# Optimization experiments

Hardware: AMD Instinct MI355X
Metric: run time of the kernel (lower is better)

The kernel has to match this reference:

```python
import jax, jax.numpy as jnp
import numpy as np

NUM_GROUPS = 32
EPS = 1e-6


def group_norm(x, gamma, beta):
    # x: (B, C, H, W), 32 groups, eps=1e-6, affine
    B, C, H, W = x.shape
    xg = x.reshape(B, NUM_GROUPS, C // NUM_GROUPS, H, W)
    mean = xg.mean(axis=(2, 3, 4), keepdims=True)
    var = xg.var(axis=(2, 3, 4), keepdims=True)
    xn = ((xg - mean) * jax.lax.rsqrt(var + EPS)).reshape(B, C, H, W)
    return xn * gamma[None, :, None, None] + beta[None, :, None, None]


def conv1x1(x, w, b):
    # 1x1 conv == channel matmul. x: (B,C,H,W), w: (O,C), b: (O,)
    return jnp.einsum('bchw,oc->bohw', x, w) + b[None, :, None, None]


def setup_inputs() -> dict:
    key = jax.random.key(0)
    B, C, H, W = 16, 512, 32, 32
    ks = jax.random.split(key, 12)
    s = 1.0 / np.sqrt(C)
    return {
        'x': jax.random.normal(ks[0], (B, C, H, W), dtype=jnp.float32),
        'gn_gamma': jnp.ones((C,), dtype=jnp.float32),
        'gn_beta': jnp.zeros((C,), dtype=jnp.float32),
        'wq': jax.random.normal(ks[1], (C, C), dtype=jnp.float32) * s,
        'bq': jnp.zeros((C,), dtype=jnp.float32),
        'wk': jax.random.normal(ks[2], (C, C), dtype=jnp.float32) * s,
        'bk': jnp.zeros((C,), dtype=jnp.float32),
        'wv': jax.random.normal(ks[3], (C, C), dtype=jnp.float32) * s,
        'bv': jnp.zeros((C,), dtype=jnp.float32),
        'wp': jax.random.normal(ks[4], (C, C), dtype=jnp.float32) * s,
        'bp': jnp.zeros((C,), dtype=jnp.float32),
    }


def reference(x, gn_gamma, gn_beta, wq, bq, wk, bk, wv, bv, wp, bp):
    B, C, H, W = x.shape
    residual = x
    xn = group_norm(x, gn_gamma, gn_beta)
    q = conv1x1(xn, wq, bq).reshape(B, C, H * W)  # (B, C, HW)
    k = conv1x1(xn, wk, bk).reshape(B, C, H * W)
    v = conv1x1(xn, wv, bv).reshape(B, C, H * W)
    scale = C ** (-0.5)
    # energy[b,i,j] = q_i . k_j
    energy = jnp.einsum('bci,bcj->bij', q, k) * scale
    attn = jax.nn.softmax(energy, axis=-1)
    # out[b,c,i] = sum_j attn[b,i,j] * v[b,c,j]
    out = jnp.einsum('bij,bcj->bci', attn, v).reshape(B, C, H, W)
    out = conv1x1(out, wp, bp)
    return out + residual
```

## Files before the change

kernel.cpp:

```cpp
#include <hip/hip_runtime.h>
#include <hip/hip_bf16.h>

using bf16 = __hip_bfloat16;

typedef __attribute__((ext_vector_type(8))) __bf16 bf16x8;
typedef __attribute__((ext_vector_type(4))) float floatx4;

#define EPS 1e-6f

#define RAW_BARRIER()  asm volatile("s_barrier" ::: "memory")
#define WAIT_VM16()    asm volatile("s_waitcnt vmcnt(16)" ::: "memory")
#define WAIT_VM8()     asm volatile("s_waitcnt vmcnt(8)" ::: "memory")
#define WAIT_VM4()     asm volatile("s_waitcnt vmcnt(4)" ::: "memory")
#define WAIT_VM0()     asm volatile("s_waitcnt vmcnt(0)" ::: "memory")
#define SCHED_FENCE()  __builtin_amdgcn_sched_barrier(0)
#define PRIO1()        __builtin_amdgcn_s_setprio(1)
#define PRIO0()        __builtin_amdgcn_s_setprio(0)

__device__ __forceinline__ void load_lds16(const void* g, void* l) {
    __builtin_amdgcn_global_load_lds(
        (const __attribute__((address_space(1))) void*)g,
        (__attribute__((address_space(3))) void*)l, 16, 0, 0);
}

__device__ __forceinline__ void storeOut(float* p, float v) { *p = v; }
__device__ __forceinline__ void storeOut(bf16* p, float v) { *p = __float2bfloat16(v); }

#define MFMA16(a, b, c) __builtin_amdgcn_mfma_f32_16x16x32_bf16(a, b, c, 0, 0, 0)

template <int BIAS_MODE, int RESID_EN, int QKV, typename OutT>
__global__ __launch_bounds__(256, 2) void gemm2b(
    const bf16* __restrict__ A, long long aStride, int lda,
    const bf16* __restrict__ B, long long bStride, int ldb,
    OutT* __restrict__ D, long long dStride, int ldd,
    bf16* __restrict__ vout, long long vStride,
    const float* __restrict__ bias,
    const float* __restrict__ resid, long long rStride, int ldr,
    int K, int tpb, int gx)
{
    constexpr int HB = 8192;
    extern __shared__ char smem[];

    const unsigned chunk = gridDim.x >> 3;
    const unsigned glob  = (blockIdx.x & 7) * chunk + (blockIdx.x >> 3);
    const unsigned z  = glob / (unsigned)tpb;
    const unsigned t  = glob % (unsigned)tpb;
    const int m0 = (int)(t / (unsigned)gx) << 7;
    const int n0 = (int)(t % (unsigned)gx) << 7;

    const int tid  = threadIdx.x;
    const int lane = tid & 63;
    const int wave = tid >> 6;
    const int wm   = wave >> 1;
    const int wn   = wave & 1;

    const bf16* Ab = A + (size_t)z * aStride + (size_t)m0 * lda;
    const bf16* Bb = B + (size_t)z * bStride + (size_t)n0 * ldb;

    floatx4 acc[4][4];
#pragma unroll
    for (int i = 0; i < 4; ++i)
#pragma unroll
        for (int j = 0; j < 4; ++j) acc[i][j] = (floatx4){0.f, 0.f, 0.f, 0.f};

    const int laneRow = lane & 15;
    const int laneKq  = lane >> 4;
    const int kqs16   = (laneKq ^ ((laneRow >> 1) & 3)) << 4;
    const int arow0   = wm * 64 + laneRow;
    const int brow0   = wn * 64 + laneRow;

    auto stage = [&](int kt, int h) {
        char* Adst = smem + ((kt & 1) * 2 + h) * HB;
        char* Bdst = smem + 4 * HB + ((kt & 1) * 2 + h) * HB;
        const int kb = (kt << 6) + (h << 5);
#pragma unroll
        for (int u = 0; u < 2; ++u) {
            const int idx = tid + u * 256;
            const int r  = idx >> 2;
            const int qs = (idx & 3) ^ ((idx >> 3) & 3);
            load_lds16(Ab + (size_t)r * lda + kb + qs * 8, Adst + idx * 16);
        }
#pragma unroll
        for (int u = 0; u < 2; ++u) {
            const int idx = tid + u * 256;
            const int r  = idx >> 2;
            const int qs = (idx & 3) ^ ((idx >> 3) & 3);
            load_lds16(Bb + (size_t)r * ldb + kb + qs * 8, Bdst + idx * 16);
        }
    };

    const int nt = K >> 6;
    stage(0, 0); stage(0, 1); stage(1, 0);

    for (int kt = 0; kt < nt; ++kt) {
        const char* Ablk = smem + (kt & 1) * 2 * HB;
        const char* Bblk = smem + 4 * HB + (kt & 1) * 2 * HB;
        const bool lastT = (kt == nt - 1);

        if (lastT) WAIT_VM4(); else WAIT_VM8();
        RAW_BARRIER();
        bf16x8 af[4], bfr[4];
#pragma unroll
        for (int im = 0; im < 4; ++im)
            af[im] = *(const bf16x8*)(Ablk + (arow0 + im * 16) * 64 + kqs16);
#pragma unroll
        for (int in = 0; in < 4; ++in)
            bfr[in] = *(const bf16x8*)(Bblk + (brow0 + in * 16) * 64 + kqs16);
        if (kt + 1 < nt) stage(kt + 1, 1);
        RAW_BARRIER();
        PRIO1();
#pragma unroll
        for (int im = 0; im < 4; ++im)
#pragma unroll
            for (int in = 0; in < 4; ++in)
                acc[im][in] = MFMA16(af[im], bfr[in], acc[im][in]);
        PRIO0();

        if (lastT) WAIT_VM0(); else WAIT_VM8();
        RAW_BARRIER();
#pragma unroll
        for (int im = 0; im < 4; ++im)
            af[im] = *(const bf16x8*)(Ablk + HB + (arow0 + im * 16) * 64 + kqs16);
#pragma unroll
        for (int in = 0; in < 4; ++in)
            bfr[in] = *(const bf16x8*)(Bblk + HB + (brow0 + in * 16) * 64 + kqs16);
        if (kt + 2 < nt) stage(kt + 2, 0);
        RAW_BARRIER();
        PRIO1();
#pragma unroll
        for (int im = 0; im < 4; ++im)
#pragma unroll
            for (int in = 0; in < 4; ++in)
                acc[im][in] = MFMA16(af[im], bfr[in], acc[im][in]);
        PRIO0();
    }

    const size_t dbase = (size_t)z * dStride;
#pragma unroll
    for (int im = 0; im < 4; ++im) {
        const int gmb = m0 + wm * 64 + im * 16 + (laneKq << 2);
#pragma unroll
        for (int in = 0; in < 4; ++in) {
            const int gn = n0 + wn * 64 + in * 16 + laneRow;
            float bn = 0.f;
            if (BIAS_MODE == 2) bn = bias[gn];
            if (QKV && n0 >= 1024) {
                union { bf16 h[4]; ushort4 u; } pk;
#pragma unroll
                for (int r = 0; r < 4; ++r)
                    pk.h[r] = __float2bfloat16(acc[im][in][r] + bn);
                *(ushort4*)(vout + (size_t)z * vStride +
                            (size_t)(gn - 1024) * 1024 + gmb) = pk.u;
            } else {
#pragma unroll
                for (int r = 0; r < 4; ++r) {
                    const int gm = gmb + r;
                    float v = acc[im][in][r];
                    if (BIAS_MODE == 1) v += bias[gm];
                    if (BIAS_MODE == 2) v += bn;
                    if (RESID_EN)
                        v += resid[(size_t)z * rStride + (size_t)gm * ldr + gn];
                    storeOut(D + dbase + (size_t)gm * ldd + gn, v);
                }
            }
        }
    }
}

__global__ __launch_bounds__(256, 1) void fattn(
    const bf16* __restrict__ qkT,
    const bf16* __restrict__ vv,
    bf16* __restrict__ O2,
    float scale)
{
    constexpr int KT = 32768;
    extern __shared__ char smem[];
    __shared__ __align__(16) char plds[4 * 1024];
    __shared__ float rsLDS[64];

    const int bid  = blockIdx.x;
    const int glob = (bid & 7) * 32 + (bid >> 3);
    const int b    = glob >> 4;
    const int i0   = (glob & 15) << 6;

    const int tid     = threadIdx.x;
    const int lane    = tid & 63;
    const int wave    = tid >> 6;
    const int laneRow = lane & 15;
    const int laneKq  = lane >> 4;
    const int kqs16   = (laneKq ^ ((laneRow >> 1) & 3)) << 4;

    const bf16* Qb = qkT + (size_t)b * 1048576 + (size_t)(i0 + wave * 16) * 1024;
    const bf16* Kb = qkT + (size_t)b * 1048576 + 512;
    const bf16* Vb = vv + (size_t)b * 524288;

    bf16x8 qf[16];
#pragma unroll
    for (int ks = 0; ks < 16; ++ks)
        qf[ks] = *(const bf16x8*)(Qb + (size_t)laneRow * 1024 + ks * 32 + laneKq * 8);

    floatx4 acc[8][4];
#pragma unroll
    for (int mf = 0; mf < 8; ++mf)
#pragma unroll
        for (int ni = 0; ni < 4; ++ni) acc[mf][ni] = (floatx4){0.f, 0.f, 0.f, 0.f};
    float rs = 0.f;

    auto stageK = [&](int jt) {
        char* dst = smem + (jt & 1) * KT;
        const bf16* src = Kb + ((size_t)jt << 5) * 1024;
#pragma unroll
        for (int u = 0; u < 8; ++u) {
            const int idx = tid + u * 256;
            const int kk = idx >> 7;
            const int j  = (idx >> 2) & 31;
            const int p  = idx & 3;
            load_lds16(src + (size_t)j * 1024 + kk * 32 + 8 * (p ^ ((j >> 1) & 3)),
                       dst + idx * 16);
        }
    };
    auto stageV = [&](int jt) {
        char* dst = smem + 2 * KT + (jt & 1) * KT;
        const bf16* src = Vb + (jt << 5);
#pragma unroll
        for (int u = 0; u < 8; ++u) {
            const int idx = tid + u * 256;
            const int c = idx >> 2;
            const int p = idx & 3;
            load_lds16(src + (size_t)c * 1024 + 8 * (p ^ ((c >> 1) & 3)),
                       dst + idx * 16);
        }
    };

    stageK(0); stageV(0); stageK(1); stageV(1);

    char* plw = plds + wave * 1024 + laneRow * 64;
    const int sw2 = ((laneRow >> 1) & 3) << 1;

    for (int jt = 0; jt < 32; ++jt) {
        if (jt == 31) WAIT_VM0(); else WAIT_VM16();
        RAW_BARRIER();
        const char* Kt = smem + (jt & 1) * KT;
        const char* Vt = smem + 2 * KT + (jt & 1) * KT;

        floatx4 s0 = (floatx4){0.f, 0.f, 0.f, 0.f};
        floatx4 s1 = (floatx4){0.f, 0.f, 0.f, 0.f};
#pragma unroll
        for (int ks = 0; ks < 16; ++ks) {
            bf16x8 kf0 = *(const bf16x8*)(Kt + ks * 2048 + laneRow * 64 + kqs16);
            bf16x8 kf1 = *(const bf16x8*)(Kt + ks * 2048 + (laneRow + 16) * 64 + kqs16);
            s0 = MFMA16(kf0, qf[ks], s0);
            s1 = MFMA16(kf1, qf[ks], s1);
        }

        union { bf16 h[4]; unsigned long long u; } w0, w1;
#pragma unroll
        for (int r = 0; r < 4; ++r) {
            float v0 = __expf(s0[r] * scale);
            float v1 = __expf(s1[r] * scale);
            rs += v0 + v1;
            w0.h[r] = __float2bfloat16(v0);
            w1.h[r] = __float2bfloat16(v1);
        }
        *(unsigned long long*)(plw + ((laneKq)     ^ sw2) * 8) = w0.u;
        *(unsigned long long*)(plw + ((laneKq + 4) ^ sw2) * 8) = w1.u;
        asm volatile("s_waitcnt lgkmcnt(0)" ::: "memory");
        RAW_BARRIER();
        SCHED_FENCE();
        bf16x8 pf[4];
#pragma unroll
        for (int ni = 0; ni < 4; ++ni)
            pf[ni] = *(const bf16x8*)(plds + ni * 1024 + laneRow * 64 + kqs16);

        PRIO1();
#pragma unroll
        for (int mf = 0; mf < 8; ++mf) {
            bf16x8 vf = *(const bf16x8*)(Vt +
                (wave * 128 + mf * 16 + laneRow) * 64 + kqs16);
#pragma unroll
            for (int ni = 0; ni < 4; ++ni)
                acc[mf][ni] = MFMA16(vf, pf[ni], acc[mf][ni]);
        }
        PRIO0();

        RAW_BARRIER();
        if (jt + 2 < 32) { stageK(jt + 2); stageV(jt + 2); }
    }

    rs += __shfl_xor(rs, 16);
    rs += __shfl_xor(rs, 32);
    if (lane < 16) rsLDS[wave * 16 + lane] = rs;
    __syncthreads();

#pragma unroll
    for (int ni = 0; ni < 4; ++ni) {
        const float ri = 1.f / rsLDS[ni * 16 + laneRow];
        bf16* Ob = O2 + (size_t)b * 524288 +
                   (size_t)(i0 + ni * 16 + laneRow) * 512 +
                   wave * 128 + (laneKq << 2);
#pragma unroll
        for (int mf = 0; mf < 8; ++mf) {
            union { bf16 h[4]; ushort4 u; } pk;
#pragma unroll
            for (int r = 0; r < 4; ++r)
                pk.h[r] = __float2bfloat16(acc[mf][ni][r] * ri);
            *(ushort4*)(Ob + mf * 16) = pk.u;
        }
    }
}

__global__ __launch_bounds__(256) void gn_stats(const float* __restrict__ x,
                                                float* __restrict__ stats)
{
    const int bg = blockIdx.x;
    const float4* p = (const float4*)(x + (size_t)bg * 16384);
    float s = 0.f, ss = 0.f;
    for (int i = threadIdx.x; i < 4096; i += 256) {
        float4 v = p[i];
        s  += v.x + v.y + v.z + v.w;
        ss += v.x * v.x + v.y * v.y + v.z * v.z + v.w * v.w;
    }
#pragma unroll
    for (int off = 32; off; off >>= 1) {
        s  += __shfl_down(s, off);
        ss += __shfl_down(ss, off);
    }
    __shared__ float rsm[4], rss[4];
    const int wv = threadIdx.x >> 6;
    if ((threadIdx.x & 63) == 0) { rsm[wv] = s; rss[wv] = ss; }
    __syncthreads();
    if (threadIdx.x == 0) {
        float S  = rsm[0] + rsm[1] + rsm[2] + rsm[3];
        float SS = rss[0] + rss[1] + rss[2] + rss[3];
        float mean = S * (1.f / 16384.f);
        float var  = SS * (1.f / 16384.f) - mean * mean;
        stats[2 * bg]     = mean;
        stats[2 * bg + 1] = rsqrtf(var + EPS);
    }
}

__global__ __launch_bounds__(256) void gn_apply_t(const float* __restrict__ x,
                                                  const float* __restrict__ stats,
                                                  const float* __restrict__ gamma,
                                                  const float* __restrict__ beta,
                                                  bf16* __restrict__ xnT)
{
    __shared__ bf16 tile[32][36];
    const int b = blockIdx.z, c0 = blockIdx.y * 32, i0 = blockIdx.x * 32;
    {
        const int cc = threadIdx.x >> 3;
        const int i4 = (threadIdx.x & 7) << 2;
        const int c  = c0 + cc;
        const float mean = stats[2 * ((b << 5) + (c >> 4))];
        const float rstd = stats[2 * ((b << 5) + (c >> 4)) + 1];
        const float a  = gamma[c] * rstd;
        const float bb = beta[c] - mean * a;
        float4 v = *(const float4*)(x + (((size_t)(b * 512 + c)) << 10) + i0 + i4);
        tile[cc][i4 + 0] = __float2bfloat16(v.x * a + bb);
        tile[cc][i4 + 1] = __float2bfloat16(v.y * a + bb);
        tile[cc][i4 + 2] = __float2bfloat16(v.z * a + bb);
        tile[cc][i4 + 3] = __float2bfloat16(v.w * a + bb);
    }
    __syncthreads();
    {
        const int ii = threadIdx.x >> 3;
        const int c4 = (threadIdx.x & 7) << 2;
        union { bf16 h[4]; uint2 u; } pk;
        pk.h[0] = tile[c4 + 0][ii];
        pk.h[1] = tile[c4 + 1][ii];
        pk.h[2] = tile[c4 + 2][ii];
        pk.h[3] = tile[c4 + 3][ii];
        *((uint2*)(xnT + (((size_t)(b * 1024 + i0 + ii)) << 9) + c0 + c4)) = pk.u;
    }
}

__global__ __launch_bounds__(256) void prep(
    const float* __restrict__ wq, const float* __restrict__ wk,
    const float* __restrict__ wv, const float* __restrict__ wp,
    bf16* __restrict__ wqkvb, bf16* __restrict__ wpb,
    const float* __restrict__ bq, const float* __restrict__ bk,
    const float* __restrict__ bv, float* __restrict__ bqkv)
{
    const int id = blockIdx.x;
    if (id < 1024) {
        const int w = id >> 8;
        const float* src = (w == 0) ? wq : (w == 1) ? wk : (w == 2) ? wv : wp;
        bf16* dst = (w < 3) ? (wqkvb + (size_t)w * 262144) : wpb;
        const int g = (id & 255) * 256 + threadIdx.x;
        float4 v = ((const float4*)src)[g];
        union { bf16 h[4]; uint2 u; } pk;
        pk.h[0] = __float2bfloat16(v.x);
        pk.h[1] = __float2bfloat16(v.y);
        pk.h[2] = __float2bfloat16(v.z);
        pk.h[3] = __float2bfloat16(v.w);
        ((uint2*)dst)[g] = pk.u;
    } else {
        for (int t = threadIdx.x; t < 1536; t += 256)
            bqkv[t] = (t < 512) ? bq[t] : (t < 1024) ? bk[t - 512] : bv[t - 1024];
    }
}

extern "C" void kernel_launch(void* const* d_in, const int* in_sizes, int n_in,
                              void* d_out, int out_size, void* d_ws, size_t ws_size,
                              hipStream_t stream)
{
    const float* x     = (const float*)d_in[0];
    const float* gamma = (const float*)d_in[1];
    const float* beta  = (const float*)d_in[2];
    const float* wq    = (const float*)d_in[3];
    const float* bq    = (const float*)d_in[4];
    const float* wk    = (const float*)d_in[5];
    const float* bk    = (const float*)d_in[6];
    const float* wv    = (const float*)d_in[7];
    const float* bv    = (const float*)d_in[8];
    const float* wp    = (const float*)d_in[9];
    const float* bp    = (const float*)d_in[10];
    float* out = (float*)d_out;

    char* ws = (char*)d_ws;
    size_t off = 0;
    auto alloc = [&](size_t bytes) -> char* {
        char* p = ws + off;
        off += (bytes + 255) & ~(size_t)255;
        return p;
    };

    const long long S  = 1024, C = 512;
    const long long BS = S * C;
    const long long ES = S * S;

    float* stats  = (float*)alloc(512 * 2 * sizeof(float));
    float* bqkv   = (float*)alloc(1536 * sizeof(float));
    bf16* wqkvb = (bf16*)alloc((size_t)3 * C * C * 2);
    bf16* wpb   = (bf16*)alloc((size_t)C * C * 2);
    bf16* xnT   = (bf16*)alloc((size_t)16 * BS * 2);
    bf16* qkT   = (bf16*)alloc((size_t)16 * ES * 2);
    bf16* vv    = (bf16*)alloc((size_t)16 * BS * 2);
    bf16* O2    = (bf16*)alloc((size_t)16 * BS * 2);

    hipFuncSetAttribute((const void*)gemm2b<2, 0, 1, bf16>,
                        hipFuncAttributeMaxDynamicSharedMemorySize, 65536);
    hipFuncSetAttribute((const void*)gemm2b<1, 1, 0, float>,
                        hipFuncAttributeMaxDynamicSharedMemorySize, 65536);
    hipFuncSetAttribute((const void*)fattn,
                        hipFuncAttributeMaxDynamicSharedMemorySize, 131072);

    prep<<<1025, 256, 0, stream>>>(wq, wk, wv, wp, wqkvb, wpb, bq, bk, bv, bqkv);

    gn_stats<<<512, 256, 0, stream>>>(x, stats);
    gn_apply_t<<<dim3(32, 16, 16), 256, 0, stream>>>(x, stats, gamma, beta, xnT);

    gemm2b<2, 0, 1, bf16><<<1536, 256, 65536, stream>>>(
        xnT, BS, 512, wqkvb, 0, 512, qkT, ES, 1024, vv, BS,
        bqkv, nullptr, 0, 0, 512, 96, 12);

    const float scale = 0.044194173824159216f;
    fattn<<<256, 256, 131072, stream>>>(qkT, vv, O2, scale);

    gemm2b<1, 1, 0, float><<<512, 256, 65536, stream>>>(
        wpb, 0, 512, O2, BS, 512, out, BS, 1024, nullptr, 0,
        bp, x, BS, 1024, 512, 32, 8);
}
```

Before: 238.5 us.

## Halve attention query tile, load V directly to registers, double occupancy

The attention kernel now processes 32 query rows per block instead of 64 and launches 512 blocks. The four waves split into two query halves and two key halves, and the softmax row sums from the two key halves are added at the end. V fragments are loaded from global memory straight into registers rather than staged through LDS, which halves dynamic shared memory to 64 KB and allows two blocks per CU. The trade is that each K tile is reused over fewer queries and V reads from global are less coalesced, in exchange for more resident waves to hide latency.

```diff
diff --git a/kernel.cpp b/kernel.cpp
--- a/kernel.cpp
+++ b/kernel.cpp
@@ -167,7 +167,7 @@
     }
 }
 
-__global__ __launch_bounds__(256, 1) void fattn(
+__global__ __launch_bounds__(256, 2) void fattn(
     const bf16* __restrict__ qkT,
     const bf16* __restrict__ vv,
     bf16* __restrict__ O2,
@@ -175,35 +175,40 @@
 {
     constexpr int KT = 32768;
     extern __shared__ char smem[];
-    __shared__ __align__(16) char plds[4 * 1024];
-    __shared__ float rsLDS[64];
+    __shared__ __align__(16) char plds[2048];
+    __shared__ float rsLDS[2][32];
 
     const int bid  = blockIdx.x;
-    const int glob = (bid & 7) * 32 + (bid >> 3);
-    const int b    = glob >> 4;
-    const int i0   = (glob & 15) << 6;
+    const int glob = (bid & 7) * 64 + (bid >> 3);
+    const int b    = glob >> 5;
+    const int i0   = (glob & 31) << 5;
 
     const int tid     = threadIdx.x;
     const int lane    = tid & 63;
     const int wave    = tid >> 6;
+    const int jh      = wave >> 1;
+    const int ih      = wave & 1;
     const int laneRow = lane & 15;
     const int laneKq  = lane >> 4;
     const int kqs16   = (laneKq ^ ((laneRow >> 1) & 3)) << 4;
-
-    const bf16* Qb = qkT + (size_t)b * 1048576 + (size_t)(i0 + wave * 16) * 1024;
+    const int sw2     = ((laneRow >> 1) & 3) << 1;
+
+    const bf16* Qb = qkT + (size_t)b * 1048576 +
+                     (size_t)(i0 + ih * 16 + laneRow) * 1024;
     const bf16* Kb = qkT + (size_t)b * 1048576 + 512;
-    const bf16* Vb = vv + (size_t)b * 524288;
+    const bf16* Vb = vv + (size_t)b * 524288 +
+                     (size_t)(wave * 128 + laneRow) * 1024 + laneKq * 8;
 
     bf16x8 qf[16];
 #pragma unroll
     for (int ks = 0; ks < 16; ++ks)
-        qf[ks] = *(const bf16x8*)(Qb + (size_t)laneRow * 1024 + ks * 32 + laneKq * 8);
-
-    floatx4 acc[8][4];
+        qf[ks] = *(const bf16x8*)(Qb + ks * 32 + laneKq * 8);
+
+    floatx4 acc[8][2];
 #pragma unroll
     for (int mf = 0; mf < 8; ++mf)
 #pragma unroll
-        for (int ni = 0; ni < 4; ++ni) acc[mf][ni] = (floatx4){0.f, 0.f, 0.f, 0.f};
+        for (int ni = 0; ni < 2; ++ni) acc[mf][ni] = (floatx4){0.f, 0.f, 0.f, 0.f};
     float rs = 0.f;
 
     auto stageK = [&](int jt) {
@@ -219,85 +224,75 @@
                        dst + idx * 16);
         }
     };
-    auto stageV = [&](int jt) {
-        char* dst = smem + 2 * KT + (jt & 1) * KT;
-        const bf16* src = Vb + (jt << 5);
-#pragma unroll
-        for (int u = 0; u < 8; ++u) {
-            const int idx = tid + u * 256;
-            const int c = idx >> 2;
-            const int p = idx & 3;
-            load_lds16(src + (size_t)c * 1024 + 8 * (p ^ ((c >> 1) & 3)),
-                       dst + idx * 16);
-        }
+
+    bf16x8 vf[8];
+    auto loadV = [&](int jt) {
+        const bf16* vs = Vb + (jt << 5);
+#pragma unroll
+        for (int mf = 0; mf < 8; ++mf)
+            vf[mf] = *(const bf16x8*)(vs + (size_t)mf * 16384);
     };
 
-    stageK(0); stageV(0); stageK(1); stageV(1);
-
-    char* plw = plds + wave * 1024 + laneRow * 64;
-    const int sw2 = ((laneRow >> 1) & 3) << 1;
+    stageK(0);
+    loadV(0);
+    SCHED_FENCE();
+    stageK(1);
 
     for (int jt = 0; jt < 32; ++jt) {
-        if (jt == 31) WAIT_VM0(); else WAIT_VM16();
+        if (jt == 31) WAIT_VM8(); else WAIT_VM16();
         RAW_BARRIER();
         const char* Kt = smem + (jt & 1) * KT;
-        const char* Vt = smem + 2 * KT + (jt & 1) * KT;
-
-        floatx4 s0 = (floatx4){0.f, 0.f, 0.f, 0.f};
-        floatx4 s1 = (floatx4){0.f, 0.f, 0.f, 0.f};
+
+        floatx4 s = (floatx4){0.f, 0.f, 0.f, 0.f};
 #pragma unroll
         for (int ks = 0; ks < 16; ++ks) {
-            bf16x8 kf0 = *(const bf16x8*)(Kt + ks * 2048 + laneRow * 64 + kqs16);
-            bf16x8 kf1 = *(const bf16x8*)(Kt + ks * 2048 + (laneRow + 16) * 64 + kqs16);
-            s0 = MFMA16(kf0, qf[ks], s0);
-            s1 = MFMA16(kf1, qf[ks], s1);
-        }
-
-        union { bf16 h[4]; unsigned long long u; } w0, w1;
+            bf16x8 kf = *(const bf16x8*)(Kt + ks * 2048 +
+                                         (jh * 16 + laneRow) * 64 + kqs16);
+            s = MFMA16(kf, qf[ks], s);
+        }
+
+        union { bf16 h[4]; unsigned long long u; } w;
 #pragma unroll
         for (int r = 0; r < 4; ++r) {
-            float v0 = __expf(s0[r] * scale);
-            float v1 = __expf(s1[r] * scale);
-            rs += v0 + v1;
-            w0.h[r] = __float2bfloat16(v0);
-            w1.h[r] = __float2bfloat16(v1);
-        }
-        *(unsigned long long*)(plw + ((laneKq)     ^ sw2) * 8) = w0.u;
-        *(unsigned long long*)(plw + ((laneKq + 4) ^ sw2) * 8) = w1.u;
+            float v = __expf(s[r] * scale);
+            rs += v;
+            w.h[r] = __float2bfloat16(v);
+        }
+        *(unsigned long long*)(plds + ih * 1024 + laneRow * 64 +
+                               (((4 * jh + laneKq)) ^ sw2) * 8) = w.u;
         asm volatile("s_waitcnt lgkmcnt(0)" ::: "memory");
         RAW_BARRIER();
         SCHED_FENCE();
-        bf16x8 pf[4];
-#pragma unroll
-        for (int ni = 0; ni < 4; ++ni)
-            pf[ni] = *(const bf16x8*)(plds + ni * 1024 + laneRow * 64 + kqs16);
+        bf16x8 pf0 = *(const bf16x8*)(plds + laneRow * 64 + kqs16);
+        bf16x8 pf1 = *(const bf16x8*)(plds + 1024 + laneRow * 64 + kqs16);
+
+        if (jt == 31) WAIT_VM0(); else WAIT_VM8();
 
         PRIO1();
 #pragma unroll
         for (int mf = 0; mf < 8; ++mf) {
-            bf16x8 vf = *(const bf16x8*)(Vt +
-                (wave * 128 + mf * 16 + laneRow) * 64 + kqs16);
-#pragma unroll
-            for (int ni = 0; ni < 4; ++ni)
-                acc[mf][ni] = MFMA16(vf, pf[ni], acc[mf][ni]);
+            acc[mf][0] = MFMA16(vf[mf], pf0, acc[mf][0]);
+            acc[mf][1] = MFMA16(vf[mf], pf1, acc[mf][1]);
         }
         PRIO0();
 
         RAW_BARRIER();
-        if (jt + 2 < 32) { stageK(jt + 2); stageV(jt + 2); }
+        if (jt + 1 < 32) loadV(jt + 1);
+        SCHED_FENCE();
+        if (jt + 2 < 32) stageK(jt + 2);
     }
 
     rs += __shfl_xor(rs, 16);
     rs += __shfl_xor(rs, 32);
-    if (lane < 16) rsLDS[wave * 16 + lane] = rs;
+    if (lane < 16) rsLDS[jh][ih * 16 + lane] = rs;
     __syncthreads();
 
 #pragma unroll
-    for (int ni = 0; ni < 4; ++ni) {
-        const float ri = 1.f / rsLDS[ni * 16 + laneRow];
+    for (int ni = 0; ni < 2; ++ni) {
+        const int row = ni * 16 + laneRow;
+        const float ri = 1.f / (rsLDS[0][row] + rsLDS[1][row]);
         bf16* Ob = O2 + (size_t)b * 524288 +
-                   (size_t)(i0 + ni * 16 + laneRow) * 512 +
-                   wave * 128 + (laneKq << 2);
+                   (size_t)(i0 + row) * 512 + wave * 128 + (laneKq << 2);
 #pragma unroll
         for (int mf = 0; mf < 8; ++mf) {
             union { bf16 h[4]; ushort4 u; } pk;
@@ -443,7 +438,7 @@
     hipFuncSetAttribute((const void*)gemm2b<1, 1, 0, float>,
                         hipFuncAttributeMaxDynamicSharedMemorySize, 65536);
     hipFuncSetAttribute((const void*)fattn,
-                        hipFuncAttributeMaxDynamicSharedMemorySize, 131072);
+                        hipFuncAttributeMaxDynamicSharedMemorySize, 65536);
 
     prep<<<1025, 256, 0, stream>>>(wq, wk, wv, wp, wqkvb, wpb, bq, bk, bv, bqkv);
 
@@ -455,7 +450,7 @@
         bqkv, nullptr, 0, 0, 512, 96, 12);
 
     const float scale = 0.044194173824159216f;
-    fattn<<<256, 256, 131072, stream>>>(qkT, vv, O2, scale);
+    fattn<<<512, 256, 65536, stream>>>(qkT, vv, O2, scale);
 
     gemm2b<1, 1, 0, float><<<512, 256, 65536, stream>>>(
         wpb, 0, 512, O2, BS, 512, out, BS, 1024, nullptr, 0,
```

Result: slower. 272.3 us (+14.2%).

## Split attention work across 8 waves per block instead of 4

Applied to the files above, without the earlier changes.

The fused attention kernel now runs 512 threads (8 waves) per block. Each wave pair splits the 32-key tile's QK^T in half and the PV output channels are spread over 8 waves, so per-wave accumulators drop from 8x4 to 4x4 fragments. Staging loads per thread halve and the vmcnt wait is adjusted to match. Row sums are combined from two halves through LDS. The aim is more latency hiding and lower register pressure, at the cost of more waves contending at the per-tile barriers and duplicated Q fragment loads.

```diff
diff --git a/kernel.cpp b/kernel.cpp
--- a/kernel.cpp
+++ b/kernel.cpp
@@ -9,7 +9,6 @@
 #define EPS 1e-6f
 
 #define RAW_BARRIER()  asm volatile("s_barrier" ::: "memory")
-#define WAIT_VM16()    asm volatile("s_waitcnt vmcnt(16)" ::: "memory")
 #define WAIT_VM8()     asm volatile("s_waitcnt vmcnt(8)" ::: "memory")
 #define WAIT_VM4()     asm volatile("s_waitcnt vmcnt(4)" ::: "memory")
 #define WAIT_VM0()     asm volatile("s_waitcnt vmcnt(0)" ::: "memory")
@@ -167,7 +166,7 @@
     }
 }
 
-__global__ __launch_bounds__(256, 1) void fattn(
+__global__ __launch_bounds__(512, 2) void fattn(
     const bf16* __restrict__ qkT,
     const bf16* __restrict__ vv,
     bf16* __restrict__ O2,
@@ -176,7 +175,7 @@
     constexpr int KT = 32768;
     extern __shared__ char smem[];
     __shared__ __align__(16) char plds[4 * 1024];
-    __shared__ float rsLDS[64];
+    __shared__ float rsLDS[2][64];
 
     const int bid  = blockIdx.x;
     const int glob = (bid & 7) * 32 + (bid >> 3);
@@ -186,22 +185,26 @@
     const int tid     = threadIdx.x;
     const int lane    = tid & 63;
     const int wave    = tid >> 6;
+    const int jh      = wave & 1;
+    const int ih      = wave >> 1;
     const int laneRow = lane & 15;
     const int laneKq  = lane >> 4;
     const int kqs16   = (laneKq ^ ((laneRow >> 1) & 3)) << 4;
-
-    const bf16* Qb = qkT + (size_t)b * 1048576 + (size_t)(i0 + wave * 16) * 1024;
+    const int sw2     = ((laneRow >> 1) & 3) << 1;
+
+    const bf16* Qb = qkT + (size_t)b * 1048576 +
+                     (size_t)(i0 + ih * 16 + laneRow) * 1024;
     const bf16* Kb = qkT + (size_t)b * 1048576 + 512;
     const bf16* Vb = vv + (size_t)b * 524288;
 
     bf16x8 qf[16];
 #pragma unroll
     for (int ks = 0; ks < 16; ++ks)
-        qf[ks] = *(const bf16x8*)(Qb + (size_t)laneRow * 1024 + ks * 32 + laneKq * 8);
-
-    floatx4 acc[8][4];
-#pragma unroll
-    for (int mf = 0; mf < 8; ++mf)
+        qf[ks] = *(const bf16x8*)(Qb + ks * 32 + laneKq * 8);
+
+    floatx4 acc[4][4];
+#pragma unroll
+    for (int mf = 0; mf < 4; ++mf)
 #pragma unroll
         for (int ni = 0; ni < 4; ++ni) acc[mf][ni] = (floatx4){0.f, 0.f, 0.f, 0.f};
     float rs = 0.f;
@@ -210,8 +213,8 @@
         char* dst = smem + (jt & 1) * KT;
         const bf16* src = Kb + ((size_t)jt << 5) * 1024;
 #pragma unroll
-        for (int u = 0; u < 8; ++u) {
-            const int idx = tid + u * 256;
+        for (int u = 0; u < 4; ++u) {
+            const int idx = tid + u * 512;
             const int kk = idx >> 7;
             const int j  = (idx >> 2) & 31;
             const int p  = idx & 3;
@@ -223,8 +226,8 @@
         char* dst = smem + 2 * KT + (jt & 1) * KT;
         const bf16* src = Vb + (jt << 5);
 #pragma unroll
-        for (int u = 0; u < 8; ++u) {
-            const int idx = tid + u * 256;
+        for (int u = 0; u < 4; ++u) {
+            const int idx = tid + u * 512;
             const int c = idx >> 2;
             const int p = idx & 3;
             load_lds16(src + (size_t)c * 1024 + 8 * (p ^ ((c >> 1) & 3)),
@@ -234,36 +237,29 @@
 
     stageK(0); stageV(0); stageK(1); stageV(1);
 
-    char* plw = plds + wave * 1024 + laneRow * 64;
-    const int sw2 = ((laneRow >> 1) & 3) << 1;
-
     for (int jt = 0; jt < 32; ++jt) {
-        if (jt == 31) WAIT_VM0(); else WAIT_VM16();
+        if (jt == 31) WAIT_VM0(); else WAIT_VM8();
         RAW_BARRIER();
         const char* Kt = smem + (jt & 1) * KT;
         const char* Vt = smem + 2 * KT + (jt & 1) * KT;
 
-        floatx4 s0 = (floatx4){0.f, 0.f, 0.f, 0.f};
-        floatx4 s1 = (floatx4){0.f, 0.f, 0.f, 0.f};
+        floatx4 s = (floatx4){0.f, 0.f, 0.f, 0.f};
 #pragma unroll
         for (int ks = 0; ks < 16; ++ks) {
-            bf16x8 kf0 = *(const bf16x8*)(Kt + ks * 2048 + laneRow * 64 + kqs16);
-            bf16x8 kf1 = *(const bf16x8*)(Kt + ks * 2048 + (laneRow + 16) * 64 + kqs16);
-            s0 = MFMA16(kf0, qf[ks], s0);
-            s1 = MFMA16(kf1, qf[ks], s1);
-        }
-
-        union { bf16 h[4]; unsigned long long u; } w0, w1;
+            bf16x8 kf = *(const bf16x8*)(Kt + ks * 2048 +
+                                         (jh * 16 + laneRow) * 64 + kqs16);
+            s = MFMA16(kf, qf[ks], s);
+        }
+
+        union { bf16 h[4]; unsigned long long u; } w;
 #pragma unroll
         for (int r = 0; r < 4; ++r) {
-            float v0 = __expf(s0[r] * scale);
-            float v1 = __expf(s1[r] * scale);
-            rs += v0 + v1;
-            w0.h[r] = __float2bfloat16(v0);
-            w1.h[r] = __float2bfloat16(v1);
-        }
-        *(unsigned long long*)(plw + ((laneKq)     ^ sw2) * 8) = w0.u;
-        *(unsigned long long*)(plw + ((laneKq + 4) ^ sw2) * 8) = w1.u;
+            float v = __expf(s[r] * scale);
+            rs += v;
+            w.h[r] = __float2bfloat16(v);
+        }
+        *(unsigned long long*)(plds + ih * 1024 + laneRow * 64 +
+                               ((4 * jh + laneKq) ^ sw2) * 8) = w.u;
         asm volatile("s_waitcnt lgkmcnt(0)" ::: "memory");
         RAW_BARRIER();
         SCHED_FENCE();
@@ -274,9 +270,9 @@
 
         PRIO1();
 #pragma unroll
-        for (int mf = 0; mf < 8; ++mf) {
+        for (int mf = 0; mf < 4; ++mf) {
             bf16x8 vf = *(const bf16x8*)(Vt +
-                (wave * 128 + mf * 16 + laneRow) * 64 + kqs16);
+                (wave * 64 + mf * 16 + laneRow) * 64 + kqs16);
 #pragma unroll
             for (int ni = 0; ni < 4; ++ni)
                 acc[mf][ni] = MFMA16(vf, pf[ni], acc[mf][ni]);
@@ -289,17 +285,17 @@
 
     rs += __shfl_xor(rs, 16);
     rs += __shfl_xor(rs, 32);
-    if (lane < 16) rsLDS[wave * 16 + lane] = rs;
+    if (lane < 16) rsLDS[jh][ih * 16 + lane] = rs;
     __syncthreads();
 
 #pragma unroll
     for (int ni = 0; ni < 4; ++ni) {
-        const float ri = 1.f / rsLDS[ni * 16 + laneRow];
+        const int row = ni * 16 + laneRow;
+        const float ri = 1.f / (rsLDS[0][row] + rsLDS[1][row]);
         bf16* Ob = O2 + (size_t)b * 524288 +
-                   (size_t)(i0 + ni * 16 + laneRow) * 512 +
-                   wave * 128 + (laneKq << 2);
-#pragma unroll
-        for (int mf = 0; mf < 8; ++mf) {
+                   (size_t)(i0 + row) * 512 + wave * 64 + (laneKq << 2);
+#pragma unroll
+        for (int mf = 0; mf < 4; ++mf) {
             union { bf16 h[4]; ushort4 u; } pk;
 #pragma unroll
             for (int r = 0; r < 4; ++r)
@@ -455,7 +451,7 @@
         bqkv, nullptr, 0, 0, 512, 96, 12);
 
     const float scale = 0.044194173824159216f;
-    fattn<<<256, 256, 131072, stream>>>(qkT, vv, O2, scale);
+    fattn<<<256, 512, 131072, stream>>>(qkT, vv, O2, scale);
 
     gemm2b<1, 1, 0, float><<<512, 256, 65536, stream>>>(
         wpb, 0, 512, O2, BS, 512, out, BS, 1024, nullptr, 0,
```

Measured after the change: 227.9 us. -4.4%, faster.
